# Optimization experiments

Measured on AMD Instinct MI355X. Metric: run time of the kernel, lower is better.

Reference implementation:

```python
import jax, jax.numpy as jnp
import numpy as np

LN_EPS = 1e-12  # BERT LayerNorm eps


def _layernorm(x, g, b):
    mu = jnp.mean(x, axis=-1, keepdims=True)
    var = jnp.mean(jnp.square(x - mu), axis=-1, keepdims=True)
    return (x - mu) * jax.lax.rsqrt(var + LN_EPS) * g + b


def setup_inputs() -> dict:
    key = jax.random.key(0)
    B, M, D, H, dh, R, Ro, Rf, F = 4, 2048, 768, 12, 64, 32, 256, 256, 3072
    ks = iter(jax.random.split(key, 32))
    n = lambda shape, s=0.02: jax.random.normal(next(ks), shape, jnp.float32) * s
    return {
        'x': jax.random.normal(next(ks), (B, M, D), jnp.float32),
        'mask': jnp.zeros((B, M), jnp.float32),  # HF-style additive mask
        'Pq': n((H, D, R)), 'Vq': n((H, R, dh)), 'bq': n((1, H, 1, dh)),
        'Pk': n((H, D, R)), 'Vk': n((H, R, dh)), 'bk': n((1, H, 1, dh)),
        'Pv': n((H, D, R)), 'Vv': n((H, R, dh)), 'bv': n((1, H, 1, dh)),
        'Uo': n((D, Ro)), 'Vo': n((Ro, D)), 'bo_attn': jnp.zeros((D,), jnp.float32),
        'U1': n((D, Rf)), 'V1': n((Rf, F)), 'b1': jnp.zeros((F,), jnp.float32),
        'U2': n((F, Rf)), 'V2': n((Rf, D)), 'b2': jnp.zeros((D,), jnp.float32),
        'ln1_g': jnp.ones((D,), jnp.float32), 'ln1_b': jnp.zeros((D,), jnp.float32),
        'ln2_g': jnp.ones((D,), jnp.float32), 'ln2_b': jnp.zeros((D,), jnp.float32),
    }


def reference(x, mask, Pq, Vq, bq, Pk, Vk, bk, Pv, Vv, bv,
              Uo, Vo, bo_attn, U1, V1, b1, U2, V2, b2,
              ln1_g, ln1_b, ln2_g, ln2_b):
    B, M, D = x.shape
    H, dh = Pq.shape[0], Vq.shape[2]
    # low-rank per-head Q/K/V: x @ P (bhmr) then @ V (bhmd) + bias
    q = jnp.einsum('bhmr,hrd->bhmd', jnp.einsum('bmd,hdr->bhmr', x, Pq), Vq) + bq
    k = jnp.einsum('bhmr,hrd->bhmd', jnp.einsum('bmd,hdr->bhmr', x, Pk), Vk) + bk
    v = jnp.einsum('bhmr,hrd->bhmd', jnp.einsum('bmd,hdr->bhmr', x, Pv), Vv) + bv
    # attention (flash_svd_attention math: scaled dot-product + additive mask)
    scores = jnp.einsum('bhmd,bhnd->bhmn', q, k) / jnp.sqrt(jnp.float32(dh))
    scores = scores + mask[:, None, None, :]
    attn = jnp.einsum('bhmn,bhnd->bhmd', jax.nn.softmax(scores, axis=-1), v)
    attn = attn.transpose(0, 2, 1, 3).reshape(B, M, D)
    # low-rank output projection + residual + LN1
    x1 = _layernorm(x + (attn @ Uo) @ Vo + bo_attn, ln1_g, ln1_b)
    # low-rank FFN (BERT intermediate: exact GELU)
    mid = x1 @ U1
    y = (jax.nn.gelu(mid @ V1 + b1, approximate=False) @ U2) @ V2 + b2
    return _layernorm(x1 + y, ln2_g, ln2_b)
```

## Files before the change

kernel.cpp:

```cpp
#include <hip/hip_runtime.h>
#include <hip/hip_bf16.h>
#include <math.h>

typedef __hip_bfloat16 bf16;
typedef __attribute__((ext_vector_type(8))) short short8;
typedef __attribute__((ext_vector_type(4))) short short4v;
typedef __attribute__((ext_vector_type(4))) float f32x4;

__device__ __forceinline__ float to_f(float x) { return x; }
__device__ __forceinline__ float to_f(bf16 x) { return __bfloat162float(x); }

template <typename T> __device__ __forceinline__ T from_f(float x);
template <> __device__ __forceinline__ float from_f<float>(float x) { return x; }
template <> __device__ __forceinline__ bf16 from_f<bf16>(float x) { return __float2bfloat16(x); }

__device__ __forceinline__ float gelu_exact(float x) {
    return 0.5f * x * (1.0f + erff(x * 0.70710678118654752f));
}

#define GLD_LDS16(g, l)                                               \
    __builtin_amdgcn_global_load_lds(                                 \
        (const __attribute__((address_space(1))) void*)(g),           \
        (__attribute__((address_space(3))) void*)(l), 16, 0, 0)

__global__ __launch_bounds__(256) void build_w_qkv_lds(const float* __restrict__ Pq,
                                                       const float* __restrict__ Vq,
                                                       const float* __restrict__ Pk,
                                                       const float* __restrict__ Vk,
                                                       const float* __restrict__ Pv,
                                                       const float* __restrict__ Vv,
                                                       bf16* __restrict__ Wt) {
    const int dt = blockIdx.x;
    const int h = blockIdx.y;
    const int which = blockIdx.z;
    const float* P = (which == 0) ? Pq : (which == 1) ? Pk : Pv;
    const float* V = (which == 0) ? Vq : (which == 1) ? Vk : Vv;
    __shared__ __align__(16) float Ps[128][36];
    __shared__ __align__(16) float Vs[32][64];
    __shared__ __align__(16) unsigned int Ot[64][68];
    const int tid = threadIdx.x;

    const float* pbase = P + ((size_t)h * 768 + dt * 128) * 32;
#pragma unroll
    for (int i = 0; i < 4; i++) {
        int idx = tid + i * 256;
        float4 v4 = ((const float4*)pbase)[idx];
        *(float4*)&Ps[idx >> 3][(idx & 7) * 4] = v4;
    }
    const float* vbase = V + (size_t)h * 2048;
#pragma unroll
    for (int i = 0; i < 2; i++) {
        int idx = tid + i * 256;
        ((float4*)&Vs[0][0])[idx] = ((const float4*)vbase)[idx];
    }
    __syncthreads();

    const int e = tid & 63, w = tid >> 6;
    float vreg[32];
#pragma unroll
    for (int r = 0; r < 32; r++) vreg[r] = Vs[r][e];

#pragma unroll
    for (int dp = 0; dp < 16; dp++) {
        const int d0 = w * 32 + dp * 2;
        float a0 = 0.f, a1 = 0.f;
#pragma unroll
        for (int r4 = 0; r4 < 8; r4++) {
            float4 p0 = *(const float4*)&Ps[d0][r4 * 4];
            float4 p1 = *(const float4*)&Ps[d0 + 1][r4 * 4];
            a0 += p0.x * vreg[r4 * 4] + p0.y * vreg[r4 * 4 + 1] + p0.z * vreg[r4 * 4 + 2] + p0.w * vreg[r4 * 4 + 3];
            a1 += p1.x * vreg[r4 * 4] + p1.y * vreg[r4 * 4 + 1] + p1.z * vreg[r4 * 4 + 2] + p1.w * vreg[r4 * 4 + 3];
        }
        unsigned int lo = (unsigned int)(unsigned short)__builtin_bit_cast(short, from_f<bf16>(a0));
        unsigned int hi = (unsigned int)(unsigned short)__builtin_bit_cast(short, from_f<bf16>(a1));
        Ot[e][w * 16 + dp] = lo | (hi << 16);
    }
    __syncthreads();

    const int erow = tid >> 2, c0 = (tid & 3) * 16;
    bf16* dst = Wt + ((size_t)which * 768 + h * 64 + erow) * 768 + dt * 128 + c0 * 2;
    *(uint4*)(dst) = *(const uint4*)&Ot[erow][c0];
    *(uint4*)(dst + 8) = *(const uint4*)&Ot[erow][c0 + 4];
    *(uint4*)(dst + 16) = *(const uint4*)&Ot[erow][c0 + 8];
    *(uint4*)(dst + 24) = *(const uint4*)&Ot[erow][c0 + 12];
}

__global__ __launch_bounds__(256) void cast_transpose_t(const float* __restrict__ in,
                                                        bf16* __restrict__ out,
                                                        int R, int Cc) {
    __shared__ float t[32][33];
    const int r0 = blockIdx.x * 32, c0 = blockIdx.y * 32;
    const int tx = threadIdx.x & 31, ty = threadIdx.x >> 5;
#pragma unroll
    for (int i = 0; i < 4; i++)
        t[ty + i * 8][tx] = in[(size_t)(r0 + ty + i * 8) * Cc + c0 + tx];
    __syncthreads();
#pragma unroll
    for (int i = 0; i < 4; i++)
        out[(size_t)(c0 + ty + i * 8) * R + r0 + tx] = from_f<bf16>(t[tx][ty + i * 8]);
}

__global__ __launch_bounds__(256) void cast_f32_bf16(const float* __restrict__ in,
                                                     bf16* __restrict__ out, int n4) {
    int t = blockIdx.x * 256 + threadIdx.x;
    if (t >= n4) return;
    float4 v = ((const float4*)in)[t];
    bf16 tmp[4] = {from_f<bf16>(v.x), from_f<bf16>(v.y), from_f<bf16>(v.z), from_f<bf16>(v.w)};
    ((short4v*)out)[t] = *(short4v*)tmp;
}

__global__ __launch_bounds__(256) void pack_bias_qkv(const float* __restrict__ bq,
                                                     const float* __restrict__ bk,
                                                     const float* __restrict__ bv,
                                                     float* __restrict__ out) {
    int t = blockIdx.x * 256 + threadIdx.x;
    if (t >= 768) return;
    out[t] = bq[t];
    out[768 + t] = bk[t];
    out[1536 + t] = bv[t];
}

template <typename TOUT, int EPI>
__global__ __launch_bounds__(256) void gemm_mfma(const bf16* __restrict__ A,
                                                 const bf16* __restrict__ Bt,
                                                 const float* __restrict__ bias,
                                                 TOUT* __restrict__ C,
                                                 int M, int N, int K) {
    __shared__ __align__(16) bf16 As[128 * 32];
    __shared__ __align__(16) bf16 Bs[128 * 32];
    const int tid = threadIdx.x;
    const int w = tid >> 6, lane = tid & 63;
    const int l = lane & 15, quad = lane >> 4;
    const int wm = w >> 1, wn = w & 1;
    const int m0 = blockIdx.x * 128, n0 = blockIdx.y * 128;

    const int r_in = lane >> 2;
    const int slot = lane & 3;
    const int rA0 = 2 * w * 16 + r_in, rA1 = rA0 + 16;
    const int q0 = slot ^ ((rA0 >> 1) & 3);
    const int q1 = slot ^ ((rA1 >> 1) & 3);
    const bf16* a0 = A + (size_t)(m0 + rA0) * K + q0 * 8;
    const bf16* a1 = A + (size_t)(m0 + rA1) * K + q1 * 8;
    const bf16* b0 = Bt + (size_t)(n0 + rA0) * K + q0 * 8;
    const bf16* b1 = Bt + (size_t)(n0 + rA1) * K + q1 * 8;
    bf16* lA0 = As + 2 * w * 512;
    bf16* lA1 = lA0 + 512;
    bf16* lB0 = Bs + 2 * w * 512;
    bf16* lB1 = lB0 + 512;

    const int swz = (quad ^ ((l >> 1) & 3)) * 8;
    f32x4 acc[4][4] = {};

    for (int k0 = 0; k0 < K; k0 += 32) {
        GLD_LDS16(a0 + k0, lA0);
        GLD_LDS16(a1 + k0, lA1);
        GLD_LDS16(b0 + k0, lB0);
        GLD_LDS16(b1 + k0, lB1);
        __syncthreads();
        short8 af[4], bfr[4];
#pragma unroll
        for (int mt = 0; mt < 4; mt++)
            af[mt] = *(const short8*)&As[(wm * 64 + mt * 16 + l) * 32 + swz];
#pragma unroll
        for (int nt = 0; nt < 4; nt++)
            bfr[nt] = *(const short8*)&Bs[(wn * 64 + nt * 16 + l) * 32 + swz];
#pragma unroll
        for (int mt = 0; mt < 4; mt++)
#pragma unroll
            for (int nt = 0; nt < 4; nt++)
                acc[mt][nt] = __builtin_amdgcn_mfma_f32_16x16x32_bf16(af[mt], bfr[nt], acc[mt][nt], 0, 0, 0);
        __syncthreads();
    }

    float bs[4];
#pragma unroll
    for (int nt = 0; nt < 4; nt++)
        bs[nt] = bias ? bias[n0 + wn * 64 + nt * 16 + l] : 0.f;
#pragma unroll
    for (int mt = 0; mt < 4; mt++) {
#pragma unroll
        for (int nt = 0; nt < 4; nt++) {
            const int col = n0 + wn * 64 + nt * 16 + l;
#pragma unroll
            for (int r = 0; r < 4; r++) {
                const int row = m0 + wm * 64 + mt * 16 + quad * 4 + r;
                float val = acc[mt][nt][r] + bs[nt];
                if (EPI == 1) val = gelu_exact(val);
                C[(size_t)row * N + col] = from_f<TOUT>(val);
            }
        }
    }
}

__global__ __launch_bounds__(256) void transpose_v(const bf16* __restrict__ qkv,
                                                   bf16* __restrict__ vt) {
    __shared__ __align__(16) bf16 t[64][72];
    const int m0 = blockIdx.x * 64;
    const int h = blockIdx.y;
    const int tid = threadIdx.x;
    const int r = tid >> 2, c0 = (tid & 3) * 16;
    {
        const size_t g = (size_t)(m0 + r) * 2304 + 1536 + h * 64 + c0;
        *(short8*)&t[r][c0] = *(const short8*)(qkv + g);
        *(short8*)&t[r][c0 + 8] = *(const short8*)(qkv + g + 8);
    }
    __syncthreads();
    const int b = m0 >> 11, mm = m0 & 2047;
    const int e = tid >> 2, mi0 = (tid & 3) * 16;
    bf16 tmp[16];
#pragma unroll
    for (int j = 0; j < 16; j++) tmp[j] = t[mi0 + j][e];
    bf16* dst = vt + (((size_t)b * 12 + h) * 64 + e) * 2048 + mm + mi0;
    *(short8*)dst = *(short8*)&tmp[0];
    *(short8*)(dst + 8) = *(short8*)&tmp[8];
}

__global__ __launch_bounds__(256, 4) void flash_attn_mfma(const bf16* __restrict__ qkv,
                                                          const bf16* __restrict__ vt,
                                                          const float* __restrict__ mask,
                                                          bf16* __restrict__ opart0,
                                                          bf16* __restrict__ opart1,
                                                          float* __restrict__ lpart) {
    const int qt = blockIdx.x, h = blockIdx.y;
    const int b = blockIdx.z >> 1, kh = blockIdx.z & 1;
    const int tid = threadIdx.x;
    const int w = tid >> 6, lane = tid & 63;
    const int l = lane & 15, quad = lane >> 4;

    __shared__ __align__(16) bf16 Ks[64 * 64];
    __shared__ __align__(16) bf16 Vs[64 * 64];
    __shared__ __align__(16) bf16 Ps[4 * 32 * 64];

    const float C1 = 0.125f * 1.44269504088896f;
    const float LOG2E = 1.44269504088896f;

    short8 qf[2][2];
#pragma unroll
    for (int mt = 0; mt < 2; mt++) {
        const int qrow = qt * 128 + w * 32 + mt * 16 + l;
        const bf16* qp = qkv + ((size_t)b * 2048 + qrow) * 2304 + h * 64 + quad * 8;
        qf[mt][0] = *(const short8*)qp;
        qf[mt][1] = *(const short8*)(qp + 32);
    }

    f32x4 of[2][4] = {};
    float lsum[2] = {0.f, 0.f};
    bf16* Pw = Ps + w * 2048;

    const int kc_end = kh * 1024 + 1024;
    for (int kc = kh * 1024; kc < kc_end; kc += 64) {
        __syncthreads();
#pragma unroll
        for (int i = 0; i < 2; i++) {
            const int cid = (w * 2 + i) * 64 + lane;
            const int row = cid >> 3, slot = cid & 7;
            const int gq = slot ^ (row & 7);
            const bf16* kp = qkv + ((size_t)b * 2048 + kc + row) * 2304 + 768 + h * 64 + gq * 8;
            GLD_LDS16(kp, &Ks[(size_t)cid * 8]);
            const bf16* vp = vt + (((size_t)b * 12 + h) * 64 + row) * 2048 + kc + gq * 8;
            GLD_LDS16(vp, &Vs[(size_t)cid * 8]);
        }
        float4 mrow[4];
#pragma unroll
        for (int nt = 0; nt < 4; nt++)
            mrow[nt] = *(const float4*)&mask[(size_t)b * 2048 + kc + nt * 16 + quad * 4];
        __syncthreads();

        f32x4 st[2][4];
#pragma unroll
        for (int nt = 0; nt < 4; nt++) {
            const int rb = (nt * 16 + l) * 64;
            short8 kf0 = *(const short8*)&Ks[rb + ((quad) ^ (l & 7)) * 8];
            short8 kf1 = *(const short8*)&Ks[rb + ((4 + quad) ^ (l & 7)) * 8];
#pragma unroll
            for (int mt = 0; mt < 2; mt++) {
                f32x4 a = {};
                a = __builtin_amdgcn_mfma_f32_16x16x32_bf16(kf0, qf[mt][0], a, 0, 0, 0);
                a = __builtin_amdgcn_mfma_f32_16x16x32_bf16(kf1, qf[mt][1], a, 0, 0, 0);
                st[mt][nt] = a;
            }
        }

        float mkl[4][4];
#pragma unroll
        for (int nt = 0; nt < 4; nt++) {
            const float* mg = (const float*)&mrow[nt];
#pragma unroll
            for (int r = 0; r < 4; r++) mkl[nt][r] = mg[r] * LOG2E;
        }

#pragma unroll
        for (int mt = 0; mt < 2; mt++) {
#pragma unroll
            for (int nt = 0; nt < 4; nt++) {
                short4v ps;
#pragma unroll
                for (int r = 0; r < 4; r++) {
                    float p = exp2f(fmaf(st[mt][nt][r], C1, mkl[nt][r]));
                    lsum[mt] += p;
                    ps[r] = __builtin_bit_cast(short, from_f<bf16>(p));
                }
                const int slot8 = (2 * nt + (quad >> 1)) ^ (l & 7);
                *(short4v*)&Pw[(mt * 16 + l) * 64 + slot8 * 8 + (quad & 1) * 4] = ps;
            }
        }

        short8 pa[2][2];
#pragma unroll
        for (int mt = 0; mt < 2; mt++)
#pragma unroll
            for (int ks = 0; ks < 2; ks++)
                pa[mt][ks] = *(const short8*)&Pw[(mt * 16 + l) * 64 + ((ks * 4 + quad) ^ (l & 7)) * 8];

#pragma unroll
        for (int nt = 0; nt < 4; nt++) {
            const int rb = (nt * 16 + l) * 64;
            short8 vf0 = *(const short8*)&Vs[rb + ((quad) ^ (l & 7)) * 8];
            short8 vf1 = *(const short8*)&Vs[rb + ((4 + quad) ^ (l & 7)) * 8];
#pragma unroll
            for (int mt = 0; mt < 2; mt++) {
                of[mt][nt] = __builtin_amdgcn_mfma_f32_16x16x32_bf16(pa[mt][0], vf0, of[mt][nt], 0, 0, 0);
                of[mt][nt] = __builtin_amdgcn_mfma_f32_16x16x32_bf16(pa[mt][1], vf1, of[mt][nt], 0, 0, 0);
            }
        }
    }

#pragma unroll
    for (int mt = 0; mt < 2; mt++) {
        lsum[mt] += __shfl_xor(lsum[mt], 16, 64);
        lsum[mt] += __shfl_xor(lsum[mt], 32, 64);
        if (lane < 16)
            lpart[(((size_t)kh * 4 + b) * 12 + h) * 2048 + qt * 128 + w * 32 + mt * 16 + lane] = lsum[mt];
    }

    bf16* op = kh ? opart1 : opart0;
#pragma unroll
    for (int mt = 0; mt < 2; mt++) {
#pragma unroll
        for (int r = 0; r < 4; r++) {
            const int row = qt * 128 + w * 32 + mt * 16 + quad * 4 + r;
#pragma unroll
            for (int nt = 0; nt < 4; nt++)
                op[((size_t)b * 2048 + row) * 768 + h * 64 + nt * 16 + l] =
                    from_f<bf16>(of[mt][nt][r]);
        }
    }
}

__global__ __launch_bounds__(256) void attn_combine(const bf16* __restrict__ o0,
                                                    const bf16* __restrict__ o1,
                                                    const float* __restrict__ lp,
                                                    bf16* __restrict__ outp) {
    const int t = blockIdx.x * 256 + threadIdx.x;
    const int col4 = t % 192;
    const int row = t / 192;
    const int b = row >> 11, m = row & 2047;
    const int h = col4 >> 4;
    const float l0 = lp[((size_t)b * 12 + h) * 2048 + m];
    const float l1 = lp[((size_t)(4 + b) * 12 + h) * 2048 + m];
    const float iv = 1.f / (l0 + l1);
    short4v a = ((const short4v*)o0)[t];
    short4v c = ((const short4v*)o1)[t];
    bf16 r[4];
#pragma unroll
    for (int i = 0; i < 4; i++) {
        float f = to_f(__builtin_bit_cast(bf16, a[i])) + to_f(__builtin_bit_cast(bf16, c[i]));
        r[i] = from_f<bf16>(f * iv);
    }
    ((short4v*)outp)[t] = *(short4v*)r;
}

template <typename TIN, typename TOUT>
__global__ __launch_bounds__(256) void ln_kernel(const TIN* __restrict__ base,
                                                 const float* __restrict__ add,
                                                 const float* __restrict__ gamma,
                                                 const float* __restrict__ beta,
                                                 TOUT* __restrict__ out) {
    const int row = blockIdx.x;
    const int tid = threadIdx.x;
    __shared__ float red[4];
    const size_t o = (size_t)row * 768;
    float v[3];
#pragma unroll
    for (int i = 0; i < 3; i++) {
        int d = tid + i * 256;
        v[i] = to_f(base[o + d]) + add[o + d];
    }
    float s = v[0] + v[1] + v[2];
#pragma unroll
    for (int off = 32; off > 0; off >>= 1) s += __shfl_down(s, off, 64);
    const int wave = tid >> 6, lane = tid & 63;
    if (lane == 0) red[wave] = s;
    __syncthreads();
    float mu = (red[0] + red[1] + red[2] + red[3]) * (1.0f / 768.0f);
    float d0 = v[0] - mu, d1 = v[1] - mu, d2 = v[2] - mu;
    float sq = d0 * d0 + d1 * d1 + d2 * d2;
    __syncthreads();
#pragma unroll
    for (int off = 32; off > 0; off >>= 1) sq += __shfl_down(sq, off, 64);
    if (lane == 0) red[wave] = sq;
    __syncthreads();
    float var = (red[0] + red[1] + red[2] + red[3]) * (1.0f / 768.0f);
    float rs = rsqrtf(var + 1e-12f);
#pragma unroll
    for (int i = 0; i < 3; i++) {
        int d = tid + i * 256;
        float y = (v[i] - mu) * rs * gamma[d] + beta[d];
        out[o + d] = from_f<TOUT>(y);
    }
}

extern "C" void kernel_launch(void* const* d_in, const int* in_sizes, int n_in,
                              void* d_out, int out_size, void* d_ws, size_t ws_size,
                              hipStream_t stream) {
    const float* x    = (const float*)d_in[0];
    const float* mask = (const float*)d_in[1];
    const float* Pq = (const float*)d_in[2];
    const float* Vq = (const float*)d_in[3];
    const float* bq = (const float*)d_in[4];
    const float* Pk = (const float*)d_in[5];
    const float* Vk = (const float*)d_in[6];
    const float* bk = (const float*)d_in[7];
    const float* Pv = (const float*)d_in[8];
    const float* Vv = (const float*)d_in[9];
    const float* bv = (const float*)d_in[10];
    const float* Uo = (const float*)d_in[11];
    const float* Vo = (const float*)d_in[12];
    const float* bo = (const float*)d_in[13];
    const float* U1 = (const float*)d_in[14];
    const float* V1 = (const float*)d_in[15];
    const float* b1 = (const float*)d_in[16];
    const float* U2 = (const float*)d_in[17];
    const float* V2 = (const float*)d_in[18];
    const float* b2 = (const float*)d_in[19];
    const float* g1 = (const float*)d_in[20];
    const float* be1 = (const float*)d_in[21];
    const float* g2 = (const float*)d_in[22];
    const float* be2 = (const float*)d_in[23];

    char* p = (char*)d_ws;
    bf16* Wqkv_t = (bf16*)p;            p += (size_t)2304 * 768 * 2;
    bf16* Wo_t   = (bf16*)p;            p += (size_t)768 * 768 * 2;
    bf16* U1t    = (bf16*)p;            p += (size_t)256 * 768 * 2;
    bf16* V1t    = (bf16*)p;            p += (size_t)3072 * 256 * 2;
    bf16* U2t    = (bf16*)p;            p += (size_t)256 * 3072 * 2;
    bf16* V2t    = (bf16*)p;            p += (size_t)768 * 256 * 2;
    float* bias_qkv = (float*)p;        p += (size_t)2304 * 4;
    bf16* xb     = (bf16*)p;
    bf16* x1b    = xb;                  p += (size_t)8192 * 768 * 2;
    bf16* qkv    = (bf16*)p;
    bf16* gbuf   = qkv;                 p += (size_t)8192 * 2304 * 2;
    bf16* vtb    = (bf16*)p;            p += (size_t)8192 * 768 * 2;
    bf16* attnb  = (bf16*)p;
    bf16* t2     = attnb;               p += (size_t)8192 * 768 * 2;
    float* bufA  = (float*)p;           p += (size_t)8192 * 768 * 4;
    bf16* t1     = (bf16*)p;            p += (size_t)8192 * 256 * 2;
    bf16* Vot = (bf16*)bufA;
    bf16* Uob = Vot + (size_t)768 * 256;
    bf16* opart1 = (bf16*)bufA;
    float* lpart = (float*)((char*)bufA + (size_t)8192 * 768 * 2);

    build_w_qkv_lds<<<dim3(6, 12, 3), 256, 0, stream>>>(Pq, Vq, Pk, Vk, Pv, Vv, Wqkv_t);
    cast_transpose_t<<<dim3(8, 24), 256, 0, stream>>>(Vo, Vot, 256, 768);
    cast_f32_bf16<<<192, 256, 0, stream>>>(Uo, Uob, 768 * 256 / 4);
    gemm_mfma<bf16, 0><<<dim3(6, 6), 256, 0, stream>>>(Vot, Uob, nullptr, Wo_t, 768, 768, 256);
    cast_transpose_t<<<dim3(24, 8), 256, 0, stream>>>(U1, U1t, 768, 256);
    cast_transpose_t<<<dim3(8, 96), 256, 0, stream>>>(V1, V1t, 256, 3072);
    cast_transpose_t<<<dim3(96, 8), 256, 0, stream>>>(U2, U2t, 3072, 256);
    cast_transpose_t<<<dim3(8, 24), 256, 0, stream>>>(V2, V2t, 256, 768);
    pack_bias_qkv<<<3, 256, 0, stream>>>(bq, bk, bv, bias_qkv);
    cast_f32_bf16<<<6144, 256, 0, stream>>>(x, xb, 8192 * 768 / 4);

    gemm_mfma<bf16, 0><<<dim3(64, 18), 256, 0, stream>>>(xb, Wqkv_t, bias_qkv, qkv, 8192, 2304, 768);

    transpose_v<<<dim3(128, 12), 256, 0, stream>>>(qkv, vtb);

    flash_attn_mfma<<<dim3(16, 12, 8), 256, 0, stream>>>(qkv, vtb, mask, attnb, opart1, lpart);
    attn_combine<<<6144, 256, 0, stream>>>(attnb, opart1, lpart, attnb);

    gemm_mfma<float, 0><<<dim3(64, 6), 256, 0, stream>>>(attnb, Wo_t, bo, bufA, 8192, 768, 768);

    ln_kernel<float, bf16><<<8192, 256, 0, stream>>>(x, bufA, g1, be1, x1b);

    gemm_mfma<bf16, 0><<<dim3(64, 2), 256, 0, stream>>>(x1b, U1t, nullptr, t1, 8192, 256, 768);

    gemm_mfma<bf16, 1><<<dim3(64, 24), 256, 0, stream>>>(t1, V1t, b1, gbuf, 8192, 3072, 256);

    gemm_mfma<bf16, 0><<<dim3(64, 2), 256, 0, stream>>>(gbuf, U2t, nullptr, t2, 8192, 256, 3072);

    gemm_mfma<float, 0><<<dim3(64, 6), 256, 0, stream>>>(t2, V2t, b2, bufA, 8192, 768, 256);

    ln_kernel<bf16, float><<<8192, 256, 0, stream>>>(x1b, bufA, g2, be2, (float*)d_out);
}
```

Measured before the change: 511.0 us.

## Double-buffer attention K/V, MFMA row sums, 64-tile narrow GEMMs, bf16 intermediates

The flash attention kernel now double-buffers K/V tiles in LDS, prefetching the next tile while the current one is computed. It also computes softmax row sums with an MFMA against a vector of ones, truncates probabilities to bf16 with byte-permute instead of rounding, and reads a mask that was scaled by log2(e) once up front. The N=256 GEMMs switch to a new 64x64-tile kernel so more blocks are launched, and the pre-LayerNorm GEMM outputs are written as bf16 instead of fp32 to cut memory traffic. In exchange it uses more LDS, and the truncation and bf16 intermediates add precision loss.

```diff
diff --git a/kernel.cpp b/kernel.cpp
--- a/kernel.cpp
+++ b/kernel.cpp
@@ -109,15 +109,20 @@
     ((short4v*)out)[t] = *(short4v*)tmp;
 }
 
-__global__ __launch_bounds__(256) void pack_bias_qkv(const float* __restrict__ bq,
-                                                     const float* __restrict__ bk,
-                                                     const float* __restrict__ bv,
-                                                     float* __restrict__ out) {
+__global__ __launch_bounds__(256) void pack_bias_mask(const float* __restrict__ bq,
+                                                      const float* __restrict__ bk,
+                                                      const float* __restrict__ bv,
+                                                      const float* __restrict__ mask,
+                                                      float* __restrict__ bias_out,
+                                                      float* __restrict__ mask2) {
     int t = blockIdx.x * 256 + threadIdx.x;
-    if (t >= 768) return;
-    out[t] = bq[t];
-    out[768 + t] = bk[t];
-    out[1536 + t] = bv[t];
+    if (t < 768) {
+        bias_out[t] = bq[t];
+        bias_out[768 + t] = bk[t];
+        bias_out[1536 + t] = bv[t];
+    }
+    int m = t - 768;
+    if (m >= 0 && m < 8192) mask2[m] = mask[m] * 1.44269504088896f;
 }
 
 template <typename TOUT, int EPI>
@@ -192,6 +197,70 @@
     }
 }
 
+template <typename TOUT, int EPI>
+__global__ __launch_bounds__(256) void gemm_mfma64(const bf16* __restrict__ A,
+                                                   const bf16* __restrict__ Bt,
+                                                   const float* __restrict__ bias,
+                                                   TOUT* __restrict__ C,
+                                                   int M, int N, int K) {
+    __shared__ __align__(16) bf16 As[64 * 32];
+    __shared__ __align__(16) bf16 Bs[64 * 32];
+    const int tid = threadIdx.x;
+    const int w = tid >> 6, lane = tid & 63;
+    const int l = lane & 15, quad = lane >> 4;
+    const int wm = w >> 1, wn = w & 1;
+    const int m0 = blockIdx.x * 64, n0 = blockIdx.y * 64;
+
+    const int cid = tid;
+    const int srow = cid >> 2, slot = cid & 3;
+    const int gq = slot ^ ((srow >> 1) & 3);
+    const bf16* ag = A + (size_t)(m0 + srow) * K + gq * 8;
+    const bf16* bg = Bt + (size_t)(n0 + srow) * K + gq * 8;
+    bf16* lA = As + w * 512;
+    bf16* lB = Bs + w * 512;
+
+    f32x4 acc[2][2] = {};
+
+    for (int k0 = 0; k0 < K; k0 += 32) {
+        GLD_LDS16(ag + k0, lA);
+        GLD_LDS16(bg + k0, lB);
+        __syncthreads();
+        short8 af[2], bfr[2];
+#pragma unroll
+        for (int mt = 0; mt < 2; mt++) {
+            const int row = wm * 32 + mt * 16 + l;
+            af[mt] = *(const short8*)&As[row * 32 + (quad ^ ((row >> 1) & 3)) * 8];
+        }
+#pragma unroll
+        for (int nt = 0; nt < 2; nt++) {
+            const int row = wn * 32 + nt * 16 + l;
+            bfr[nt] = *(const short8*)&Bs[row * 32 + (quad ^ ((row >> 1) & 3)) * 8];
+        }
+#pragma unroll
+        for (int mt = 0; mt < 2; mt++)
+#pragma unroll
+            for (int nt = 0; nt < 2; nt++)
+                acc[mt][nt] = __builtin_amdgcn_mfma_f32_16x16x32_bf16(af[mt], bfr[nt], acc[mt][nt], 0, 0, 0);
+        __syncthreads();
+    }
+
+#pragma unroll
+    for (int mt = 0; mt < 2; mt++) {
+#pragma unroll
+        for (int nt = 0; nt < 2; nt++) {
+            const int col = n0 + wn * 32 + nt * 16 + l;
+            const float bsv = bias ? bias[col] : 0.f;
+#pragma unroll
+            for (int r = 0; r < 4; r++) {
+                const int row = m0 + wm * 32 + mt * 16 + quad * 4 + r;
+                float val = acc[mt][nt][r] + bsv;
+                if (EPI == 1) val = gelu_exact(val);
+                C[(size_t)row * N + col] = from_f<TOUT>(val);
+            }
+        }
+    }
+}
+
 __global__ __launch_bounds__(256) void transpose_v(const bf16* __restrict__ qkv,
                                                    bf16* __restrict__ vt) {
     __shared__ __align__(16) bf16 t[64][72];
@@ -217,7 +286,7 @@
 
 __global__ __launch_bounds__(256, 4) void flash_attn_mfma(const bf16* __restrict__ qkv,
                                                           const bf16* __restrict__ vt,
-                                                          const float* __restrict__ mask,
+                                                          const float* __restrict__ mask2,
                                                           bf16* __restrict__ opart0,
                                                           bf16* __restrict__ opart1,
                                                           float* __restrict__ lpart) {
@@ -227,12 +296,11 @@
     const int w = tid >> 6, lane = tid & 63;
     const int l = lane & 15, quad = lane >> 4;
 
-    __shared__ __align__(16) bf16 Ks[64 * 64];
-    __shared__ __align__(16) bf16 Vs[64 * 64];
+    __shared__ __align__(16) bf16 Ks[2][64 * 64];
+    __shared__ __align__(16) bf16 Vs[2][64 * 64];
     __shared__ __align__(16) bf16 Ps[4 * 32 * 64];
 
     const float C1 = 0.125f * 1.44269504088896f;
-    const float LOG2E = 1.44269504088896f;
 
     short8 qf[2][2];
 #pragma unroll
@@ -243,35 +311,49 @@
         qf[mt][1] = *(const short8*)(qp + 32);
     }
 
+    short8 ones;
+#pragma unroll
+    for (int i = 0; i < 8; i++) ones[i] = (short)0x3F80;
+
     f32x4 of[2][4] = {};
-    float lsum[2] = {0.f, 0.f};
+    f32x4 lacc[2] = {};
     bf16* Pw = Ps + w * 2048;
 
-    const int kc_end = kh * 1024 + 1024;
-    for (int kc = kh * 1024; kc < kc_end; kc += 64) {
-        __syncthreads();
+    auto stage = [&](int kc, int buf) {
 #pragma unroll
         for (int i = 0; i < 2; i++) {
             const int cid = (w * 2 + i) * 64 + lane;
             const int row = cid >> 3, slot = cid & 7;
             const int gq = slot ^ (row & 7);
             const bf16* kp = qkv + ((size_t)b * 2048 + kc + row) * 2304 + 768 + h * 64 + gq * 8;
-            GLD_LDS16(kp, &Ks[(size_t)cid * 8]);
+            GLD_LDS16(kp, &Ks[buf][(size_t)cid * 8]);
             const bf16* vp = vt + (((size_t)b * 12 + h) * 64 + row) * 2048 + kc + gq * 8;
-            GLD_LDS16(vp, &Vs[(size_t)cid * 8]);
-        }
+            GLD_LDS16(vp, &Vs[buf][(size_t)cid * 8]);
+        }
+    };
+
+    const int kc0 = kh * 1024;
+    int cur = 0;
+    stage(kc0, 0);
+
+    for (int it = 0; it < 16; it++) {
+        const int kc = kc0 + it * 64;
+        __syncthreads();
         float4 mrow[4];
 #pragma unroll
         for (int nt = 0; nt < 4; nt++)
-            mrow[nt] = *(const float4*)&mask[(size_t)b * 2048 + kc + nt * 16 + quad * 4];
-        __syncthreads();
+            mrow[nt] = *(const float4*)&mask2[(size_t)b * 2048 + kc + nt * 16 + quad * 4];
+        if (it < 15) stage(kc + 64, cur ^ 1);
+
+        const bf16* Kc = Ks[cur];
+        const bf16* Vc = Vs[cur];
 
         f32x4 st[2][4];
 #pragma unroll
         for (int nt = 0; nt < 4; nt++) {
             const int rb = (nt * 16 + l) * 64;
-            short8 kf0 = *(const short8*)&Ks[rb + ((quad) ^ (l & 7)) * 8];
-            short8 kf1 = *(const short8*)&Ks[rb + ((4 + quad) ^ (l & 7)) * 8];
+            short8 kf0 = *(const short8*)&Kc[rb + ((quad) ^ (l & 7)) * 8];
+            short8 kf1 = *(const short8*)&Kc[rb + ((4 + quad) ^ (l & 7)) * 8];
 #pragma unroll
             for (int mt = 0; mt < 2; mt++) {
                 f32x4 a = {};
@@ -281,27 +363,22 @@
             }
         }
 
-        float mkl[4][4];
-#pragma unroll
-        for (int nt = 0; nt < 4; nt++) {
-            const float* mg = (const float*)&mrow[nt];
-#pragma unroll
-            for (int r = 0; r < 4; r++) mkl[nt][r] = mg[r] * LOG2E;
-        }
-
 #pragma unroll
         for (int mt = 0; mt < 2; mt++) {
 #pragma unroll
             for (int nt = 0; nt < 4; nt++) {
-                short4v ps;
-#pragma unroll
-                for (int r = 0; r < 4; r++) {
-                    float p = exp2f(fmaf(st[mt][nt][r], C1, mkl[nt][r]));
-                    lsum[mt] += p;
-                    ps[r] = __builtin_bit_cast(short, from_f<bf16>(p));
-                }
+                const float* mg = (const float*)&mrow[nt];
+                float p0 = exp2f(fmaf(st[mt][nt][0], C1, mg[0]));
+                float p1 = exp2f(fmaf(st[mt][nt][1], C1, mg[1]));
+                float p2 = exp2f(fmaf(st[mt][nt][2], C1, mg[2]));
+                float p3 = exp2f(fmaf(st[mt][nt][3], C1, mg[3]));
+                unsigned d0 = __builtin_amdgcn_perm(__builtin_bit_cast(unsigned, p1),
+                                                    __builtin_bit_cast(unsigned, p0), 0x07060302u);
+                unsigned d1 = __builtin_amdgcn_perm(__builtin_bit_cast(unsigned, p3),
+                                                    __builtin_bit_cast(unsigned, p2), 0x07060302u);
                 const int slot8 = (2 * nt + (quad >> 1)) ^ (l & 7);
-                *(short4v*)&Pw[(mt * 16 + l) * 64 + slot8 * 8 + (quad & 1) * 4] = ps;
+                uint2 u = {d0, d1};
+                *(uint2*)&Pw[(mt * 16 + l) * 64 + slot8 * 8 + (quad & 1) * 4] = u;
             }
         }
 
@@ -313,24 +390,33 @@
                 pa[mt][ks] = *(const short8*)&Pw[(mt * 16 + l) * 64 + ((ks * 4 + quad) ^ (l & 7)) * 8];
 
 #pragma unroll
+        for (int mt = 0; mt < 2; mt++) {
+            lacc[mt] = __builtin_amdgcn_mfma_f32_16x16x32_bf16(pa[mt][0], ones, lacc[mt], 0, 0, 0);
+            lacc[mt] = __builtin_amdgcn_mfma_f32_16x16x32_bf16(pa[mt][1], ones, lacc[mt], 0, 0, 0);
+        }
+
+#pragma unroll
         for (int nt = 0; nt < 4; nt++) {
             const int rb = (nt * 16 + l) * 64;
-            short8 vf0 = *(const short8*)&Vs[rb + ((quad) ^ (l & 7)) * 8];
-            short8 vf1 = *(const short8*)&Vs[rb + ((4 + quad) ^ (l & 7)) * 8];
+            short8 vf0 = *(const short8*)&Vc[rb + ((quad) ^ (l & 7)) * 8];
+            short8 vf1 = *(const short8*)&Vc[rb + ((4 + quad) ^ (l & 7)) * 8];
 #pragma unroll
             for (int mt = 0; mt < 2; mt++) {
                 of[mt][nt] = __builtin_amdgcn_mfma_f32_16x16x32_bf16(pa[mt][0], vf0, of[mt][nt], 0, 0, 0);
                 of[mt][nt] = __builtin_amdgcn_mfma_f32_16x16x32_bf16(pa[mt][1], vf1, of[mt][nt], 0, 0, 0);
             }
         }
+        cur ^= 1;
     }
 
 #pragma unroll
     for (int mt = 0; mt < 2; mt++) {
-        lsum[mt] += __shfl_xor(lsum[mt], 16, 64);
-        lsum[mt] += __shfl_xor(lsum[mt], 32, 64);
-        if (lane < 16)
-            lpart[(((size_t)kh * 4 + b) * 12 + h) * 2048 + qt * 128 + w * 32 + mt * 16 + lane] = lsum[mt];
+        if (l == 0) {
+#pragma unroll
+            for (int r = 0; r < 4; r++)
+                lpart[(((size_t)kh * 4 + b) * 12 + h) * 2048 + qt * 128 + w * 32 + mt * 16 + quad * 4 + r] =
+                    lacc[mt][r];
+        }
     }
 
     bf16* op = kh ? opart1 : opart0;
@@ -370,9 +456,9 @@
     ((short4v*)outp)[t] = *(short4v*)r;
 }
 
-template <typename TIN, typename TOUT>
+template <typename TIN, typename TADD, typename TOUT>
 __global__ __launch_bounds__(256) void ln_kernel(const TIN* __restrict__ base,
-                                                 const float* __restrict__ add,
+                                                 const TADD* __restrict__ add,
                                                  const float* __restrict__ gamma,
                                                  const float* __restrict__ beta,
                                                  TOUT* __restrict__ out) {
@@ -384,7 +470,7 @@
 #pragma unroll
     for (int i = 0; i < 3; i++) {
         int d = tid + i * 256;
-        v[i] = to_f(base[o + d]) + add[o + d];
+        v[i] = to_f(base[o + d]) + to_f(add[o + d]);
     }
     float s = v[0] + v[1] + v[2];
 #pragma unroll
@@ -446,6 +532,7 @@
     bf16* U2t    = (bf16*)p;            p += (size_t)256 * 3072 * 2;
     bf16* V2t    = (bf16*)p;            p += (size_t)768 * 256 * 2;
     float* bias_qkv = (float*)p;        p += (size_t)2304 * 4;
+    float* mask2 = (float*)p;           p += (size_t)8192 * 4;
     bf16* xb     = (bf16*)p;
     bf16* x1b    = xb;                  p += (size_t)8192 * 768 * 2;
     bf16* qkv    = (bf16*)p;
@@ -453,12 +540,14 @@
     bf16* vtb    = (bf16*)p;            p += (size_t)8192 * 768 * 2;
     bf16* attnb  = (bf16*)p;
     bf16* t2     = attnb;               p += (size_t)8192 * 768 * 2;
-    float* bufA  = (float*)p;           p += (size_t)8192 * 768 * 4;
+    char* regR   = p;                   p += (size_t)8192 * 768 * 4;
     bf16* t1     = (bf16*)p;            p += (size_t)8192 * 256 * 2;
-    bf16* Vot = (bf16*)bufA;
+    bf16* Vot = (bf16*)regR;
     bf16* Uob = Vot + (size_t)768 * 256;
-    bf16* opart1 = (bf16*)bufA;
-    float* lpart = (float*)((char*)bufA + (size_t)8192 * 768 * 2);
+    bf16* opart1 = (bf16*)regR;
+    float* lpart = (float*)(regR + (size_t)8192 * 768 * 2);
+    bf16* y1b = (bf16*)regR;
+    bf16* y2b = (bf16*)(regR + (size_t)8192 * 768 * 2);
 
     build_w_qkv_lds<<<dim3(6, 12, 3), 256, 0, stream>>>(Pq, Vq, Pk, Vk, Pv, Vv, Wqkv_t);
     cast_transpose_t<<<dim3(8, 24), 256, 0, stream>>>(Vo, Vot, 256, 768);
@@ -468,27 +557,27 @@
     cast_transpose_t<<<dim3(8, 96), 256, 0, stream>>>(V1, V1t, 256, 3072);
     cast_transpose_t<<<dim3(96, 8), 256, 0, stream>>>(U2, U2t, 3072, 256);
     cast_transpose_t<<<dim3(8, 24), 256, 0, stream>>>(V2, V2t, 256, 768);
-    pack_bias_qkv<<<3, 256, 0, stream>>>(bq, bk, bv, bias_qkv);
+    pack_bias_mask<<<35, 256, 0, stream>>>(bq, bk, bv, mask, bias_qkv, mask2);
     cast_f32_bf16<<<6144, 256, 0, stream>>>(x, xb, 8192 * 768 / 4);
 
     gemm_mfma<bf16, 0><<<dim3(64, 18), 256, 0, stream>>>(xb, Wqkv_t, bias_qkv, qkv, 8192, 2304, 768);
 
     transpose_v<<<dim3(128, 12), 256, 0, stream>>>(qkv, vtb);
 
-    flash_attn_mfma<<<dim3(16, 12, 8), 256, 0, stream>>>(qkv, vtb, mask, attnb, opart1, lpart);
+    flash_attn_mfma<<<dim3(16, 12, 8), 256, 0, stream>>>(qkv, vtb, mask2, attnb, opart1, lpart);
     attn_combine<<<6144, 256, 0, stream>>>(attnb, opart1, lpart, attnb);
 
-    gemm_mfma<float, 0><<<dim3(64, 6), 256, 0, stream>>>(attnb, Wo_t, bo, bufA, 8192, 768, 768);
-
-    ln_kernel<float, bf16><<<8192, 256, 0, stream>>>(x, bufA, g1, be1, x1b);
-
-    gemm_mfma<bf16, 0><<<dim3(64, 2), 256, 0, stream>>>(x1b, U1t, nullptr, t1, 8192, 256, 768);
+    gemm_mfma<bf16, 0><<<dim3(64, 6), 256, 0, stream>>>(attnb, Wo_t, bo, y1b, 8192, 768, 768);
+
+    ln_kernel<float, bf16, bf16><<<8192, 256, 0, stream>>>(x, y1b, g1, be1, x1b);
+
+    gemm_mfma64<bf16, 0><<<dim3(128, 4), 256, 0, stream>>>(x1b, U1t, nullptr, t1, 8192, 256, 768);
 
     gemm_mfma<bf16, 1><<<dim3(64, 24), 256, 0, stream>>>(t1, V1t, b1, gbuf, 8192, 3072, 256);
 
-    gemm_mfma<bf16, 0><<<dim3(64, 2), 256, 0, stream>>>(gbuf, U2t, nullptr, t2, 8192, 256, 3072);
-
-    gemm_mfma<float, 0><<<dim3(64, 6), 256, 0, stream>>>(t2, V2t, b2, bufA, 8192, 768, 256);
-
-    ln_kernel<bf16, float><<<8192, 256, 0, stream>>>(x1b, bufA, g2, be2, (float*)d_out);
-}
+    gemm_mfma64<bf16, 0><<<dim3(128, 4), 256, 0, stream>>>(gbuf, U2t, nullptr, t2, 8192, 256, 3072);
+
+    gemm_mfma<bf16, 0><<<dim3(64, 6), 256, 0, stream>>>(t2, V2t, b2, y2b, 8192, 768, 256);
+
+    ln_kernel<bf16, bf16, float><<<8192, 256, 0, stream>>>(x1b, y2b, g2, be2, (float*)d_out);
+}
```

Result: faster. 430.6 us (-15.7%).
